# Optimization experiments

Measured on AMD Instinct MI355X. Metric: run time of the kernel, lower is better.

Reference implementation:

```python
import jax, jax.numpy as jnp
import numpy as np

B, NEG = 4, 33          # queries, candidates per query
N, R = 10000, 256       # entities, relation types (even; R//2 direct)
D, L = 64, 6            # hidden dim, conv layers
E, ER = 200000, 80000   # entity edges, edges per relation graph (hh/ht/th/tt)
F = 2 * D
EPS = 1e-5


def _ln(x, s, b):
    m = jnp.mean(x, -1, keepdims=True)
    v = jnp.mean((x - m) ** 2, -1, keepdims=True)
    return (x - m) * jax.lax.rsqrt(v + EPS) * s + b


def _conv(x, boundary, relation, src, dst, etype, p):
    # GeneralizedRelationalConv (dependent=False, project_relations=True):
    # distmult message, sum aggregate + boundary self-loop, update=relu(LN(Linear([x,agg])))
    p1w, p1b, p2w, p2b, lw, lb, lns, lnb = p
    rel = jax.nn.relu(relation @ p1w + p1b) @ p2w + p2b     # relation projection MLP
    msg = x[:, src, :] * rel[:, etype, :]                   # [B, Eg, D] gathered messages
    agg = jnp.zeros_like(boundary).at[:, dst, :].add(msg) + boundary
    out = jnp.concatenate([x, agg], -1) @ lw + lb
    return jax.nn.relu(_ln(out, lns, lnb))


def _entity_bf(rel_reps, h0, r0, src, dst, etype, params):
    # NBFNet Bellman-Ford over the entity graph, query-conditioned boundary
    q = rel_reps[jnp.arange(B), r0]                         # [B, D]
    boundary = jnp.zeros((B, N, D), q.dtype).at[jnp.arange(B), h0].add(q)
    x = boundary
    for i in range(L):
        x = _conv(x, boundary, rel_reps, src, dst, etype,
                  tuple(t[i] for t in params)) + x          # short_cut residual
    nq = jnp.broadcast_to(q[:, None, :], (B, N, D))
    return jnp.concatenate([x, nq], -1)                     # [B, N, 2D]


def _forward(floats, ints):
    (e1p1w, e1p1b, e1p2w, e1p2b, e1lw, e1lb, e1lns, e1lnb,
     e2p1w, e2p1b, e2p2w, e2p2b, e2lw, e2lb, e2lns, e2lnb,
     e2m1w, e2m1b, e2m2w, e2m2b,
     rp1w, rp1b, rp2w, rp2b, rlw, rlb, rlns, rlnb, nmw, nmb) = floats
    edge_src, edge_dst, edge_type, rel_src, rel_dst, rel_etype, batch = ints
    h0 = batch[:, 0, 0]
    t_idx = batch[:, :, 1]
    r0 = batch[:, 0, 2]
    e1p = (e1p1w, e1p1b, e1p2w, e1p2b, e1lw, e1lb, e1lns, e1lnb)
    # ---- RelNet over the 4 relation graphs (nodes=relations, edge types=entities) ----
    node_reps = jnp.ones((B, N, D), e1p1w.dtype)
    q = jnp.ones((B, D), e1p1w.dtype)
    boundary = jnp.zeros((B, R, D), q.dtype).at[jnp.arange(B), r0].add(q)
    x = boundary
    for i in range(L):
        h = sum(_conv(x, boundary, node_reps, rel_src[g], rel_dst[g], rel_etype[g],
                      (rp1w[g, i], rp1b[g, i], rp2w[g, i], rp2b[g, i],
                       rlw[g, i], rlb[g, i], rlns[g, i], rlnb[g, i]))
                for g in range(4))
        x = h + x                                           # short_cut
        if i == 0:
            # entity_model_1 refreshes the per-entity (relation-graph edge type) reps
            feat = _entity_bf(x, h0, r0, edge_src, edge_dst, edge_type, e1p)
            node_reps = feat @ nmw + nmb                    # [B, N, D]
    rel_reps = x                                            # [B, R, D]
    # ---- EntityNet 2: score candidates ----
    e2p = (e2p1w, e2p1b, e2p2w, e2p2b, e2lw, e2lb, e2lns, e2lnb)
    feat2 = _entity_bf(rel_reps, h0, r0, edge_src, edge_dst, edge_type, e2p)
    g = jnp.take_along_axis(feat2, jnp.broadcast_to(t_idx[:, :, None], (B, NEG, F)), axis=1)
    score = (jax.nn.relu(g @ e2m1w + e2m1b) @ e2m2w + e2m2b)[..., 0]
    return score                                            # [B, NEG]


def setup_inputs():
    key = jax.random.key(0)
    ks = iter(jax.random.split(key, 64))
    def w(shape, std=0.08):
        return jax.random.normal(next(ks), shape, jnp.float32) * std
    inp = {}
    inp["edge_src"] = jax.random.randint(next(ks), (E,), 0, N, jnp.int32)
    inp["edge_dst"] = jax.random.randint(next(ks), (E,), 0, N, jnp.int32)
    inp["edge_type"] = jax.random.randint(next(ks), (E,), 0, R, jnp.int32)
    inp["rel_src"] = jax.random.randint(next(ks), (4, ER), 0, R, jnp.int32)
    inp["rel_dst"] = jax.random.randint(next(ks), (4, ER), 0, R, jnp.int32)
    inp["rel_etype"] = jax.random.randint(next(ks), (4, ER), 0, N, jnp.int32)
    h = jax.random.randint(next(ks), (B, 1), 0, N, jnp.int32)
    t = jax.random.randint(next(ks), (B, NEG), 0, N, jnp.int32)
    r = jax.random.randint(next(ks), (B, 1), 0, R // 2, jnp.int32)
    inp["batch"] = jnp.stack([jnp.broadcast_to(h, (B, NEG)), t,
                              jnp.broadcast_to(r, (B, NEG))], -1)
    for pre in ("e1", "e2"):
        inp[pre + "p1w"] = w((L, D, D)); inp[pre + "p1b"] = jnp.zeros((L, D))
        inp[pre + "p2w"] = w((L, D, D)); inp[pre + "p2b"] = jnp.zeros((L, D))
        inp[pre + "lw"] = w((L, F, D));  inp[pre + "lb"] = jnp.zeros((L, D))
        inp[pre + "lns"] = jnp.ones((L, D)); inp[pre + "lnb"] = jnp.zeros((L, D))
    inp["e2m1w"] = w((F, F)); inp["e2m1b"] = jnp.zeros((F,))
    inp["e2m2w"] = w((F, 1)); inp["e2m2b"] = jnp.zeros((1,))
    inp["rp1w"] = w((4, L, D, D)); inp["rp1b"] = jnp.zeros((4, L, D))
    inp["rp2w"] = w((4, L, D, D)); inp["rp2b"] = jnp.zeros((4, L, D))
    inp["rlw"] = w((4, L, F, D));  inp["rlb"] = jnp.zeros((4, L, D))
    inp["rlns"] = jnp.ones((4, L, D)); inp["rlnb"] = jnp.zeros((4, L, D))
    inp["nmw"] = w((F, D)); inp["nmb"] = jnp.zeros((D,))
    return inp


def reference(e1p1w, e1p1b, e1p2w, e1p2b, e1lw, e1lb, e1lns, e1lnb,
              e2p1w, e2p1b, e2p2w, e2p2b, e2lw, e2lb, e2lns, e2lnb,
              e2m1w, e2m1b, e2m2w, e2m2b,
              rp1w, rp1b, rp2w, rp2b, rlw, rlb, rlns, rlnb, nmw, nmb,
              edge_src, edge_dst, edge_type, rel_src, rel_dst, rel_etype, batch):
    floats = (e1p1w, e1p1b, e1p2w, e1p2b, e1lw, e1lb, e1lns, e1lnb,
              e2p1w, e2p1b, e2p2w, e2p2b, e2lw, e2lb, e2lns, e2lnb,
              e2m1w, e2m1b, e2m2w, e2m2b,
              rp1w, rp1b, rp2w, rp2b, rlw, rlb, rlns, rlnb, nmw, nmb)
    ints = (edge_src, edge_dst, edge_type, rel_src, rel_dst, rel_etype, batch)
    return _forward(floats, ints)
```

## Files before the change

kernel.cpp:

```cpp
#include <hip/hip_runtime.h>

constexpr int kB   = 4;
constexpr int kNEG = 33;
constexpr int kN   = 10000;
constexpr int kR   = 256;
constexpr int kD   = 64;
constexpr int kL   = 6;
constexpr int kE   = 200000;
constexpr int kER  = 80000;

typedef const float* fp;
typedef __attribute__((ext_vector_type(8))) short bf16x8;
typedef __attribute__((ext_vector_type(4))) float f32x4;

__device__ __forceinline__ float rdlane(float v, int l) {
  return __uint_as_float(__builtin_amdgcn_readlane(__float_as_uint(v), l));
}
__device__ __forceinline__ float wave_sum64(float v) {
  #pragma unroll
  for (int o = 32; o > 0; o >>= 1) v += __shfl_xor(v, o, 64);
  return v;
}
__device__ __forceinline__ short f2bf(float x) {
  unsigned u = __float_as_uint(x);
  unsigned r = (u + 0x7fffu + ((u >> 16) & 1u)) >> 16;
  return (short)r;
}
__device__ __forceinline__ float bf2f_u(unsigned short s) {
  return __uint_as_float(((unsigned)s) << 16);
}
__device__ __forceinline__ float bf2f(short s) { return bf2f_u((unsigned short)s); }

__global__ void k_fill(float* __restrict__ p, float v, int n) {
  int i = blockIdx.x * blockDim.x + threadIdx.x;
  int stride = gridDim.x * blockDim.x;
  for (; i < n; i += stride) p[i] = v;
}
__global__ void k_zero_i(int* __restrict__ p, int n) {
  int i = blockIdx.x * blockDim.x + threadIdx.x;
  int stride = gridDim.x * blockDim.x;
  for (; i < n; i += stride) p[i] = 0;
}
__global__ void k_add_row(float* __restrict__ dst, const int* __restrict__ batch) {
  int tid = threadIdx.x;
  int b = tid >> 6, d = tid & 63;
  int row = batch[b * kNEG * 3 + 2];
  dst[((size_t)b * kR + row) * 64 + d] += 1.0f;
}
__global__ void k_get_q(float* __restrict__ q, const float* __restrict__ relx,
                        const int* __restrict__ batch) {
  int tid = threadIdx.x;
  int b = tid >> 6, d = tid & 63;
  int r0 = batch[b * kNEG * 3 + 2];
  q[b * 64 + d] = relx[((size_t)b * kR + r0) * 64 + d];
}

__global__ void k_hist(const int* __restrict__ dst, int ne, int* __restrict__ cnt) {
  int i = blockIdx.x * blockDim.x + threadIdx.x;
  if (i < ne) atomicAdd(&cnt[dst[i]], 1);
}
__global__ void k_hist_rel(const int* __restrict__ rel_dst, int* __restrict__ cnt) {
  int g = blockIdx.y;
  int i = blockIdx.x * blockDim.x + threadIdx.x;
  if (i < kER) atomicAdd(&cnt[g * 256 + rel_dst[(size_t)g * kER + i]], 1);
}
__global__ void k_scan_multi(const int* __restrict__ cnt, int* __restrict__ start,
                             int* __restrict__ cursor, int n, int cstride, int sstride) {
  const int* c = cnt + (size_t)blockIdx.x * cstride;
  int* st = start + (size_t)blockIdx.x * sstride;
  int* cu = cursor + (size_t)blockIdx.x * sstride;
  __shared__ int part[256];
  int t = threadIdx.x;
  int chunk = (n + 255) / 256;
  int lo = t * chunk, hi = min(lo + chunk, n);
  int s = 0;
  for (int i = lo; i < hi; ++i) s += c[i];
  part[t] = s;
  __syncthreads();
  if (t == 0) { int run = 0; for (int i = 0; i < 256; ++i) { int v = part[i]; part[i] = run; run += v; } }
  __syncthreads();
  int run = part[t];
  for (int i = lo; i < hi; ++i) { st[i] = run; cu[i] = run; run += c[i]; }
  if (t == 255) st[n] = run;
}
__global__ void k_fill_csr(const int* __restrict__ src, const int* __restrict__ dst,
                           const int* __restrict__ et, int ne,
                           int* __restrict__ cursor, int2* __restrict__ out) {
  int i = blockIdx.x * blockDim.x + threadIdx.x;
  if (i < ne) {
    int p = atomicAdd(&cursor[dst[i]], 1);
    out[p] = make_int2(src[i], et[i]);
  }
}
__global__ void k_fill_csr_rel(const int* __restrict__ src, const int* __restrict__ dst,
                               const int* __restrict__ et,
                               int* __restrict__ cursor, int2* __restrict__ out) {
  int g = blockIdx.y;
  int i = blockIdx.x * blockDim.x + threadIdx.x;
  if (i < kER) {
    int p = atomicAdd(&cursor[g * 257 + dst[(size_t)g * kER + i]], 1);
    out[(size_t)g * kER + p] = make_int2(src[(size_t)g * kER + i], et[(size_t)g * kER + i]);
  }
}

__global__ void k_packw(const float* __restrict__ w1, const float* __restrict__ w2,
                        short* __restrict__ w1h, short* __restrict__ w1l,
                        short* __restrict__ w2h, short* __restrict__ w2l) {
  int pg = blockIdx.x;
  for (int i = threadIdx.x; i < 4096; i += 256) {
    int t = i & 7, lane = (i >> 3) & 63, nt = (i >> 9) & 3, ks = i >> 11;
    int mr = lane & 15, kg = lane >> 4;
    int src = pg * 4096 + (ks * 32 + kg * 8 + t) * 64 + nt * 16 + mr;
    int dst = pg * 4096 + i;
    float v1 = w1[src]; short h1 = f2bf(v1);
    w1h[dst] = h1; w1l[dst] = f2bf(v1 - bf2f(h1));
    float v2 = w2[src]; short h2 = f2bf(v2);
    w2h[dst] = h2; w2l[dst] = f2bf(v2 - bf2f(h2));
  }
}

__global__ void __launch_bounds__(256) k_mlp_mfma(
    const float* __restrict__ in, const short* __restrict__ w1h, const short* __restrict__ w1l,
    const float* __restrict__ b1, const short* __restrict__ w2h, const short* __restrict__ w2l,
    const float* __restrict__ b2, int layer, unsigned short* __restrict__ out) {
  int g = blockIdx.y;
  int pg = g * kL + layer;
  int w = threadIdx.x >> 6, lane = threadIdx.x & 63;
  int mrow = lane & 15, kgrp = lane >> 4;
  int r0 = blockIdx.x * 64 + w * 16;
  __shared__ float hbuf[4][16][68];
  const float* xp = in + (size_t)(r0 + mrow) * 64 + kgrp * 8;
  bf16x8 a1h[2], a1l[2];
  #pragma unroll
  for (int ks = 0; ks < 2; ++ks) {
    #pragma unroll
    for (int t = 0; t < 8; ++t) {
      float v = xp[ks * 32 + t];
      short h = f2bf(v); a1h[ks][t] = h; a1l[ks][t] = f2bf(v - bf2f(h));
    }
  }
  const bf16x8* B1h = (const bf16x8*)(w1h + (size_t)pg * 4096);
  const bf16x8* B1l = (const bf16x8*)(w1l + (size_t)pg * 4096);
  #pragma unroll
  for (int nt = 0; nt < 4; ++nt) {
    f32x4 c = {0.f, 0.f, 0.f, 0.f};
    #pragma unroll
    for (int ks = 0; ks < 2; ++ks) {
      bf16x8 bh = B1h[(ks * 4 + nt) * 64 + lane];
      bf16x8 bl = B1l[(ks * 4 + nt) * 64 + lane];
      c = __builtin_amdgcn_mfma_f32_16x16x32_bf16(a1h[ks], bh, c, 0, 0, 0);
      c = __builtin_amdgcn_mfma_f32_16x16x32_bf16(a1h[ks], bl, c, 0, 0, 0);
      c = __builtin_amdgcn_mfma_f32_16x16x32_bf16(a1l[ks], bh, c, 0, 0, 0);
    }
    int col = nt * 16 + mrow;
    float bv = b1[pg * 64 + col];
    #pragma unroll
    for (int rg = 0; rg < 4; ++rg)
      hbuf[w][kgrp * 4 + rg][col] = fmaxf(c[rg] + bv, 0.f);
  }
  __syncthreads();
  bf16x8 a2h[2], a2l[2];
  #pragma unroll
  for (int ks = 0; ks < 2; ++ks) {
    #pragma unroll
    for (int t = 0; t < 8; ++t) {
      float v = hbuf[w][mrow][ks * 32 + kgrp * 8 + t];
      short h = f2bf(v); a2h[ks][t] = h; a2l[ks][t] = f2bf(v - bf2f(h));
    }
  }
  const bf16x8* B2h = (const bf16x8*)(w2h + (size_t)pg * 4096);
  const bf16x8* B2l = (const bf16x8*)(w2l + (size_t)pg * 4096);
  unsigned short* ob = out + (size_t)g * kB * kN * 64;
  #pragma unroll
  for (int nt = 0; nt < 4; ++nt) {
    f32x4 c = {0.f, 0.f, 0.f, 0.f};
    #pragma unroll
    for (int ks = 0; ks < 2; ++ks) {
      bf16x8 bh = B2h[(ks * 4 + nt) * 64 + lane];
      bf16x8 bl = B2l[(ks * 4 + nt) * 64 + lane];
      c = __builtin_amdgcn_mfma_f32_16x16x32_bf16(a2h[ks], bh, c, 0, 0, 0);
      c = __builtin_amdgcn_mfma_f32_16x16x32_bf16(a2h[ks], bl, c, 0, 0, 0);
      c = __builtin_amdgcn_mfma_f32_16x16x32_bf16(a2l[ks], bh, c, 0, 0, 0);
    }
    int col = nt * 16 + mrow;
    float bv = b2[pg * 64 + col];
    #pragma unroll
    for (int rg = 0; rg < 4; ++rg)
      ob[(size_t)(r0 + kgrp * 4 + rg) * 64 + col] = (unsigned short)f2bf(c[rg] + bv);
  }
}

__global__ void __launch_bounds__(256) k_mlp_rel6(
    const float* __restrict__ in, fp p1w, fp p1b, fp p2w, fp p2b,
    float* __restrict__ out) {
  int j = blockIdx.y;
  int row = blockIdx.x * 4 + (threadIdx.x >> 6);
  int lane = threadIdx.x & 63;
  fp W1 = p1w + (size_t)j * 4096;
  fp W2 = p2w + (size_t)j * 4096;
  float xv = in[(size_t)row * 64 + lane];
  float a = p1b[j * 64 + lane];
  float wbuf[8];
  #pragma unroll
  for (int kk = 0; kk < 64; kk += 8) {
    #pragma unroll
    for (int u = 0; u < 8; ++u) wbuf[u] = W1[(kk + u) * 64 + lane];
    #pragma unroll
    for (int u = 0; u < 8; ++u) a = fmaf(rdlane(xv, kk + u), wbuf[u], a);
  }
  a = fmaxf(a, 0.f);
  float c = p2b[j * 64 + lane];
  #pragma unroll
  for (int kk = 0; kk < 64; kk += 8) {
    #pragma unroll
    for (int u = 0; u < 8; ++u) wbuf[u] = W2[(kk + u) * 64 + lane];
    #pragma unroll
    for (int u = 0; u < 8; ++u) c = fmaf(rdlane(a, kk + u), wbuf[u], c);
  }
  out[((size_t)j * kB * kR + row) * 64 + lane] = c;
}

__global__ void k_gate0(fp p1w, fp p1b, fp p2w, fp p2b, float* __restrict__ gate0) {
  int g = threadIdx.x >> 6, lane = threadIdx.x & 63;
  int pg = g * kL;
  float a = p1b[pg * 64 + lane];
  #pragma unroll
  for (int k = 0; k < 64; ++k) a += p1w[(size_t)pg * 4096 + k * 64 + lane];
  a = fmaxf(a, 0.f);
  float c = p2b[pg * 64 + lane];
  #pragma unroll
  for (int k = 0; k < 64; ++k)
    c = fmaf(rdlane(a, k), p2w[(size_t)pg * 4096 + k * 64 + lane], c);
  gate0[g * 64 + lane] = c;
}
__global__ void k_rel_agg0(const int* __restrict__ rel_start, const int2* __restrict__ rel_edges,
                           const int* __restrict__ batch, const float* __restrict__ gate0,
                           float* __restrict__ agg) {
  int wid = (blockIdx.x * blockDim.x + threadIdx.x) >> 6;
  int lane = threadIdx.x & 63;
  int g = wid >> 10, rem = wid & 1023, b = rem >> 8, r = rem & 255;
  int r0 = batch[b * kNEG * 3 + 2];
  const int* start = rel_start + g * 257;
  const int2* edges = rel_edges + (size_t)g * kER;
  int s0 = start[r], s1 = start[r + 1];
  int cnt = 0;
  for (int base = s0; base < s1; base += 64) {
    int e = base + lane;
    bool m = false;
    if (e < s1) m = (edges[e].x == r0);
    cnt += (int)__popcll(__ballot(m));
  }
  agg[(size_t)wid * 64 + lane] = gate0[g * 64 + lane] * (float)cnt + ((r == r0) ? 1.f : 0.f);
}

__global__ void __launch_bounds__(256) k_gather_rel_all(
    const float* __restrict__ x, const unsigned short* __restrict__ gateN,
    const int* __restrict__ rel_start, const int2* __restrict__ rel_edges,
    const int* __restrict__ batch, float* __restrict__ agg) {
  int i = blockIdx.x;
  int s = i & 15, r = i >> 4;
  int g = s >> 2, b = s & 3;
  const unsigned short* gate = gateN + (size_t)g * kB * kN * 64;
  const int* start = rel_start + g * 257;
  const int2* edges = rel_edges + (size_t)g * kER;
  int w = threadIdx.x >> 6, lane = threadIdx.x & 63;
  const float* xb = x + (size_t)b * kR * 64 + lane;
  const unsigned short* gb = gate + (size_t)b * kN * 64 + lane;
  int s0 = start[r], s1 = start[r + 1];
  int len = s1 - s0;
  int per = (len + 3) >> 2;
  int e0 = s0 + w * per, e1 = min(e0 + per, s1);
  float acc = 0.f;
  int2 se;
  if (e0 < e1) se = edges[e0];
  for (int e = e0; e < e1; ++e) {
    int2 cur = se;
    if (e + 1 < e1) se = edges[e + 1];
    acc = fmaf(xb[(size_t)cur.x * 64], bf2f_u(gb[(size_t)cur.y * 64]), acc);
  }
  __shared__ float red[4][64];
  red[w][lane] = acc;
  __syncthreads();
  if (w == 0) {
    float a = red[0][lane] + red[1][lane] + red[2][lane] + red[3][lane];
    int r0 = batch[b * kNEG * 3 + 2];
    if (r == r0) a += 1.0f;
    agg[((size_t)g * kB * kR + b * kR + r) * 64 + lane] = a;
  }
}

__global__ void __launch_bounds__(256) k_conv_rel2(
    float* __restrict__ rel_x, const float* __restrict__ agg,
    fp rlw, fp rlb, fp rlns, fp rlnb, int layer) {
  int row = blockIdx.x;
  int g = threadIdx.x >> 6, lane = threadIdx.x & 63;
  int pg = g * kL + layer;
  float xr = rel_x[(size_t)row * 64 + lane];
  float ag = agg[((size_t)g * kB * kR + row) * 64 + lane];
  fp w1 = rlw + (size_t)pg * 8192;
  float o = rlb[pg * 64 + lane];
  float wbuf[8];
  #pragma unroll
  for (int kk = 0; kk < 128; kk += 8) {
    #pragma unroll
    for (int u = 0; u < 8; ++u) wbuf[u] = w1[(kk + u) * 64 + lane];
    #pragma unroll
    for (int u = 0; u < 8; ++u) {
      int k = kk + u;
      float xv = (k < 64) ? rdlane(xr, k) : rdlane(ag, k - 64);
      o = fmaf(xv, wbuf[u], o);
    }
  }
  float m = wave_sum64(o) * (1.f / 64.f);
  float c = o - m;
  float v = wave_sum64(c * c) * (1.f / 64.f);
  float y = fmaxf(c * rsqrtf(v + 1e-5f) * rlns[pg * 64 + lane] + rlnb[pg * 64 + lane], 0.f);
  __shared__ float red[4][64];
  red[g][lane] = y;
  __syncthreads();
  if (g == 0)
    rel_x[(size_t)row * 64 + lane] = xr + red[0][lane] + red[1][lane] + red[2][lane] + red[3][lane];
}

template<bool FIRST>
__global__ void __launch_bounds__(256) k_ent_layer2(
    const float* __restrict__ xcur, float* __restrict__ xnext,
    const unsigned short* __restrict__ xbf_cur, unsigned short* __restrict__ xbf_next,
    const float* __restrict__ gateL,
    const int* __restrict__ start, const int2* __restrict__ edges,
    const float* __restrict__ q, const int* __restrict__ batch,
    fp lw, fp lb, fp lns, fp lnb) {
  int n = (blockIdx.x * blockDim.x + threadIdx.x) >> 6;
  if (n >= kN) return;
  int lane = threadIdx.x & 63;
  int h0[4]; float qv[4];
  #pragma unroll
  for (int b = 0; b < 4; ++b) { h0[b] = batch[b * kNEG * 3]; qv[b] = q[b * 64 + lane]; }
  float a0 = 0.f, a1 = 0.f, a2 = 0.f, a3 = 0.f;
  int s0 = start[n], s1 = start[n + 1];
  int2 se;
  if (s0 < s1) se = edges[s0];
  for (int e = s0; e < s1; ++e) {
    int2 cur = se;
    if (e + 1 < s1) se = edges[e + 1];
    const float* gp = gateL + (size_t)cur.y * 64 + lane;
    if (FIRST) {
      if (cur.x == h0[0]) a0 = fmaf(qv[0], gp[0],     a0);
      if (cur.x == h0[1]) a1 = fmaf(qv[1], gp[16384], a1);
      if (cur.x == h0[2]) a2 = fmaf(qv[2], gp[32768], a2);
      if (cur.x == h0[3]) a3 = fmaf(qv[3], gp[49152], a3);
    } else {
      const unsigned short* xp = xbf_cur + (size_t)cur.x * 64 + lane;
      a0 = fmaf(bf2f_u(xp[0]),       gp[0],     a0);
      a1 = fmaf(bf2f_u(xp[640000]),  gp[16384], a1);
      a2 = fmaf(bf2f_u(xp[1280000]), gp[32768], a2);
      a3 = fmaf(bf2f_u(xp[1920000]), gp[49152], a3);
    }
  }
  if (n == h0[0]) a0 += qv[0];
  if (n == h0[1]) a1 += qv[1];
  if (n == h0[2]) a2 += qv[2];
  if (n == h0[3]) a3 += qv[3];
  float x0, x1, x2, x3;
  if (FIRST) {
    x0 = (n == h0[0]) ? qv[0] : 0.f; x1 = (n == h0[1]) ? qv[1] : 0.f;
    x2 = (n == h0[2]) ? qv[2] : 0.f; x3 = (n == h0[3]) ? qv[3] : 0.f;
  } else {
    const float* xp = xcur + (size_t)n * 64 + lane;
    x0 = xp[0]; x1 = xp[640000]; x2 = xp[1280000]; x3 = xp[1920000];
  }
  float bv = lb[lane];
  float o0 = bv, o1 = bv, o2 = bv, o3 = bv;
  float wbuf[8];
  #pragma unroll
  for (int kk = 0; kk < 128; kk += 8) {
    #pragma unroll
    for (int u = 0; u < 8; ++u) wbuf[u] = lw[(kk + u) * 64 + lane];
    #pragma unroll
    for (int u = 0; u < 8; ++u) {
      int k = kk + u; float w = wbuf[u];
      if (k < 64) {
        o0 = fmaf(rdlane(x0, k), w, o0); o1 = fmaf(rdlane(x1, k), w, o1);
        o2 = fmaf(rdlane(x2, k), w, o2); o3 = fmaf(rdlane(x3, k), w, o3);
      } else {
        o0 = fmaf(rdlane(a0, k - 64), w, o0); o1 = fmaf(rdlane(a1, k - 64), w, o1);
        o2 = fmaf(rdlane(a2, k - 64), w, o2); o3 = fmaf(rdlane(a3, k - 64), w, o3);
      }
    }
  }
  float s = lns[lane], t = lnb[lane];
  float* yp = xnext + (size_t)n * 64 + lane;
  unsigned short* mp = xbf_next + (size_t)n * 64 + lane;
  { float m = wave_sum64(o0) * (1.f/64.f); float c = o0 - m;
    float v = wave_sum64(c*c) * (1.f/64.f);
    float y = x0 + fmaxf(c * rsqrtf(v + 1e-5f) * s + t, 0.f);
    yp[0] = y; mp[0] = (unsigned short)f2bf(y); }
  { float m = wave_sum64(o1) * (1.f/64.f); float c = o1 - m;
    float v = wave_sum64(c*c) * (1.f/64.f);
    float y = x1 + fmaxf(c * rsqrtf(v + 1e-5f) * s + t, 0.f);
    yp[640000] = y; mp[640000] = (unsigned short)f2bf(y); }
  { float m = wave_sum64(o2) * (1.f/64.f); float c = o2 - m;
    float v = wave_sum64(c*c) * (1.f/64.f);
    float y = x2 + fmaxf(c * rsqrtf(v + 1e-5f) * s + t, 0.f);
    yp[1280000] = y; mp[1280000] = (unsigned short)f2bf(y); }
  { float m = wave_sum64(o3) * (1.f/64.f); float c = o3 - m;
    float v = wave_sum64(c*c) * (1.f/64.f);
    float y = x3 + fmaxf(c * rsqrtf(v + 1e-5f) * s + t, 0.f);
    yp[1920000] = y; mp[1920000] = (unsigned short)f2bf(y); }
}

__global__ void __launch_bounds__(256) k_nodeup4(
    const float* __restrict__ x, const float* __restrict__ q,
    fp nmw, fp nmb, float* __restrict__ out) {
  int wid = (blockIdx.x * blockDim.x + threadIdx.x) >> 6;
  int lane = threadIdx.x & 63;
  int r0 = wid * 4;
  if (r0 >= kB * kN) return;
  int b = r0 / kN;
  const float* ip = x + (size_t)r0 * 64 + lane;
  float x0 = ip[0], x1 = ip[64], x2 = ip[128], x3 = ip[192];
  float qv = q[b * 64 + lane];
  float bv = nmb[lane];
  float c0 = bv, c1 = bv, c2 = bv, c3 = bv;
  float wbuf[4];
  #pragma unroll
  for (int kk = 0; kk < 64; kk += 4) {
    #pragma unroll
    for (int u = 0; u < 4; ++u) wbuf[u] = nmw[(kk + u) * 64 + lane];
    #pragma unroll
    for (int u = 0; u < 4; ++u) {
      int k = kk + u; float w = wbuf[u];
      c0 = fmaf(rdlane(x0, k), w, c0); c1 = fmaf(rdlane(x1, k), w, c1);
      c2 = fmaf(rdlane(x2, k), w, c2); c3 = fmaf(rdlane(x3, k), w, c3);
    }
  }
  float qa = 0.f;
  #pragma unroll
  for (int k = 0; k < 64; ++k)
    qa = fmaf(rdlane(qv, k), nmw[(64 + k) * 64 + lane], qa);
  float* op = out + (size_t)r0 * 64 + lane;
  op[0] = c0 + qa; op[64] = c1 + qa; op[128] = c2 + qa; op[192] = c3 + qa;
}

__global__ void k_score(const float* __restrict__ entx, const float* __restrict__ q,
                        const int* __restrict__ batch,
                        fp m1w, fp m1b, fp m2w, fp m2b,
                        float* __restrict__ out) {
  int b = blockIdx.x / kNEG, n = blockIdx.x % kNEG;
  int t = batch[(b * kNEG + n) * 3 + 1];
  int j = threadIdx.x;
  __shared__ float gv[128];
  __shared__ float red[2];
  gv[j] = (j < 64) ? entx[((size_t)b * kN + t) * 64 + j] : q[b * 64 + (j - 64)];
  __syncthreads();
  float acc = m1b[j];
  #pragma unroll 16
  for (int k = 0; k < 128; ++k)
    acc = fmaf(gv[k], m1w[k * 128 + j], acc);
  float h = fmaxf(acc, 0.f) * m2w[j];
  h = wave_sum64(h);
  if ((j & 63) == 0) red[j >> 6] = h;
  __syncthreads();
  if (j == 0) out[b * kNEG + n] = red[0] + red[1] + m2b[0];
}

extern "C" void kernel_launch(void* const* d_in, const int* in_sizes, int n_in,
                              void* d_out, int out_size, void* d_ws, size_t ws_size,
                              hipStream_t stream) {
  const int* edge_src  = (const int*)d_in[0];
  const int* edge_dst  = (const int*)d_in[1];
  const int* edge_type = (const int*)d_in[2];
  const int* rel_src   = (const int*)d_in[3];
  const int* rel_dst   = (const int*)d_in[4];
  const int* rel_etype = (const int*)d_in[5];
  const int* batch     = (const int*)d_in[6];
  fp e1p1w = (fp)d_in[7],  e1p1b = (fp)d_in[8],  e1p2w = (fp)d_in[9],  e1p2b = (fp)d_in[10];
  fp e1lw  = (fp)d_in[11], e1lb  = (fp)d_in[12], e1lns = (fp)d_in[13], e1lnb = (fp)d_in[14];
  fp e2p1w = (fp)d_in[15], e2p1b = (fp)d_in[16], e2p2w = (fp)d_in[17], e2p2b = (fp)d_in[18];
  fp e2lw  = (fp)d_in[19], e2lb  = (fp)d_in[20], e2lns = (fp)d_in[21], e2lnb = (fp)d_in[22];
  fp e2m1w = (fp)d_in[23], e2m1b = (fp)d_in[24], e2m2w = (fp)d_in[25], e2m2b = (fp)d_in[26];
  fp rp1w  = (fp)d_in[27], rp1b  = (fp)d_in[28], rp2w  = (fp)d_in[29], rp2b  = (fp)d_in[30];
  fp rlw   = (fp)d_in[31], rlb   = (fp)d_in[32], rlns  = (fp)d_in[33], rlnb  = (fp)d_in[34];
  fp nmw   = (fp)d_in[35], nmb   = (fp)d_in[36];

  float* ws = (float*)d_ws;
  float* rel_x     = ws;
  float* q         = rel_x + 65536;
  float* gate0     = q + 256;
  float* gateR6    = gate0 + 256;
  float* rel_agg   = gateR6 + 393216;
  float* node_reps = rel_agg + 262144;
  float* ent_xa    = node_reps + 2560000;
  float* ent_xb    = ent_xa + 2560000;
  unsigned short* gateN  = (unsigned short*)(ent_xb + 2560000);
  unsigned short* ent_ba = gateN + 10240000;
  unsigned short* ent_bb = ent_ba + 2560000;
  int*   iws       = (int*)(ent_bb + 2560000);
  int2*  ent_edges = (int2*)iws;
  int2*  rel_edges = (int2*)(iws + 400000);
  int*   ent_cnt   = iws + 400000 + 640000;
  int*   ent_start = ent_cnt + 10000;
  int*   ent_cur   = ent_start + 10001;
  int*   rel_cnt   = ent_cur + 10001;
  int*   rel_start = rel_cnt + 1024;
  int*   rel_cur   = rel_start + 1028;
  short* w1hp      = (short*)(rel_cur + 1028 + 2);
  short* w1lp      = w1hp + 98304;
  short* w2hp      = w1lp + 98304;
  short* w2lp      = w2hp + 98304;

  const int nZero = 10000 + 10001 + 10001 + 1024;
  k_zero_i<<<(nZero + 255) / 256, 256, 0, stream>>>(ent_cnt, nZero);
  k_hist<<<(kE + 255) / 256, 256, 0, stream>>>(edge_dst, kE, ent_cnt);
  k_hist_rel<<<dim3((kER + 255) / 256, 4), 256, 0, stream>>>(rel_dst, rel_cnt);
  k_scan_multi<<<1, 256, 0, stream>>>(ent_cnt, ent_start, ent_cur, 10000, 0, 0);
  k_scan_multi<<<4, 256, 0, stream>>>(rel_cnt, rel_start, rel_cur, 256, 256, 257);
  k_fill_csr<<<(kE + 255) / 256, 256, 0, stream>>>(edge_src, edge_dst, edge_type, kE, ent_cur, ent_edges);
  k_fill_csr_rel<<<dim3((kER + 255) / 256, 4), 256, 0, stream>>>(rel_src, rel_dst, rel_etype, rel_cur, rel_edges);
  k_packw<<<24, 256, 0, stream>>>(rp1w, rp2w, w1hp, w1lp, w2hp, w2lp);

  k_fill<<<256, 256, 0, stream>>>(rel_x, 0.f, kB * kR * kD);
  k_add_row<<<1, 256, 0, stream>>>(rel_x, batch);

  k_gate0<<<1, 256, 0, stream>>>(rp1w, rp1b, rp2w, rp2b, gate0);
  k_rel_agg0<<<1024, 256, 0, stream>>>(rel_start, rel_edges, batch, gate0, rel_agg);
  k_conv_rel2<<<1024, 256, 0, stream>>>(rel_x, rel_agg, rlw, rlb, rlns, rlnb, 0);

  k_get_q<<<1, 256, 0, stream>>>(q, rel_x, batch);
  k_mlp_rel6<<<dim3(256, 6), 256, 0, stream>>>(rel_x, e1p1w, e1p1b, e1p2w, e1p2b, gateR6);
  {
    float* cur = ent_xa; float* nxt = ent_xb;
    unsigned short* bcur = ent_ba; unsigned short* bnxt = ent_bb;
    for (int j = 0; j < kL; ++j) {
      const float* gL = gateR6 + (size_t)j * kB * kR * 64;
      if (j == 0)
        k_ent_layer2<true><<<2500, 256, 0, stream>>>(cur, nxt, bcur, bnxt, gL, ent_start, ent_edges, q, batch,
            e1lw + (size_t)j * 8192, e1lb + (size_t)j * 64, e1lns + (size_t)j * 64, e1lnb + (size_t)j * 64);
      else
        k_ent_layer2<false><<<2500, 256, 0, stream>>>(cur, nxt, bcur, bnxt, gL, ent_start, ent_edges, q, batch,
            e1lw + (size_t)j * 8192, e1lb + (size_t)j * 64, e1lns + (size_t)j * 64, e1lnb + (size_t)j * 64);
      float* tf = cur; cur = nxt; nxt = tf;
      unsigned short* tb = bcur; bcur = bnxt; bnxt = tb;
    }
    k_nodeup4<<<2500, 256, 0, stream>>>(cur, q, nmw, nmb, node_reps);
  }

  for (int i = 1; i < kL; ++i) {
    k_mlp_mfma<<<dim3(625, 4), 256, 0, stream>>>(node_reps, w1hp, w1lp, rp1b, w2hp, w2lp, rp2b, i, gateN);
    k_gather_rel_all<<<4096, 256, 0, stream>>>(rel_x, gateN, rel_start, rel_edges, batch, rel_agg);
    k_conv_rel2<<<1024, 256, 0, stream>>>(rel_x, rel_agg, rlw, rlb, rlns, rlnb, i);
  }

  k_get_q<<<1, 256, 0, stream>>>(q, rel_x, batch);
  k_mlp_rel6<<<dim3(256, 6), 256, 0, stream>>>(rel_x, e2p1w, e2p1b, e2p2w, e2p2b, gateR6);
  {
    float* cur = ent_xa; float* nxt = ent_xb;
    unsigned short* bcur = ent_ba; unsigned short* bnxt = ent_bb;
    for (int j = 0; j < kL; ++j) {
      const float* gL = gateR6 + (size_t)j * kB * kR * 64;
      if (j == 0)
        k_ent_layer2<true><<<2500, 256, 0, stream>>>(cur, nxt, bcur, bnxt, gL, ent_start, ent_edges, q, batch,
            e2lw + (size_t)j * 8192, e2lb + (size_t)j * 64, e2lns + (size_t)j * 64, e2lnb + (size_t)j * 64);
      else
        k_ent_layer2<false><<<2500, 256, 0, stream>>>(cur, nxt, bcur, bnxt, gL, ent_start, ent_edges, q, batch,
            e2lw + (size_t)j * 8192, e2lb + (size_t)j * 64, e2lns + (size_t)j * 64, e2lnb + (size_t)j * 64);
      float* tf = cur; cur = nxt; nxt = tf;
      unsigned short* tb = bcur; bcur = bnxt; bnxt = tb;
    }
    k_score<<<kB * kNEG, 128, 0, stream>>>(cur, q, batch, e2m1w, e2m1b, e2m2w, e2m2b, (float*)d_out);
  }
}
```

Before: 1.198 ms.

## Interleave batch dimension in gathered tensors and store relation gates as bf16

The gathered operands (the entity bf16 mirror, the per-layer relation gates, the relation-net gate outputs and a new relation-state mirror) are switched from batch-major to node-major layout with the 4 batch rows adjacent. One edge gather then touches a single contiguous 512-byte or 1 KB region instead of four regions far apart. The relation gather kernel now handles all four batches per block, which cuts its grid from 4096 to 1024 blocks and removes repeated edge-list reads. The entity gates are also stored as bf16, which adds rounding error. Keeping the batch-interleaved relation-state mirror costs an extra write in the conv kernel, and the unused k_mirror_relx kernel is added but never launched.

```diff
diff --git a/kernel.cpp b/kernel.cpp
--- a/kernel.cpp
+++ b/kernel.cpp
@@ -46,6 +46,11 @@
   int b = tid >> 6, d = tid & 63;
   int row = batch[b * kNEG * 3 + 2];
   dst[((size_t)b * kR + row) * 64 + d] += 1.0f;
+}
+__global__ void k_mirror_relx(const float* __restrict__ rel_x, float* __restrict__ rxi) {
+  int i = blockIdx.x * blockDim.x + threadIdx.x;
+  int d = i & 63, r = (i >> 6) & 255, b = i >> 14;
+  rxi[((size_t)r * 4 + b) * 64 + d] = rel_x[i];
 }
 __global__ void k_get_q(float* __restrict__ q, const float* __restrict__ relx,
                         const int* __restrict__ batch) {
@@ -185,14 +190,18 @@
     int col = nt * 16 + mrow;
     float bv = b2[pg * 64 + col];
     #pragma unroll
-    for (int rg = 0; rg < 4; ++rg)
-      ob[(size_t)(r0 + kgrp * 4 + rg) * 64 + col] = (unsigned short)f2bf(c[rg] + bv);
+    for (int rg = 0; rg < 4; ++rg) {
+      int grow = r0 + kgrp * 4 + rg;
+      int bb = grow / kN;
+      int nn = grow - bb * kN;
+      ob[((size_t)nn * 4 + bb) * 64 + col] = (unsigned short)f2bf(c[rg] + bv);
+    }
   }
 }
 
 __global__ void __launch_bounds__(256) k_mlp_rel6(
     const float* __restrict__ in, fp p1w, fp p1b, fp p2w, fp p2b,
-    float* __restrict__ out) {
+    unsigned short* __restrict__ out) {
   int j = blockIdx.y;
   int row = blockIdx.x * 4 + (threadIdx.x >> 6);
   int lane = threadIdx.x & 63;
@@ -217,7 +226,8 @@
     #pragma unroll
     for (int u = 0; u < 8; ++u) c = fmaf(rdlane(a, kk + u), wbuf[u], c);
   }
-  out[((size_t)j * kB * kR + row) * 64 + lane] = c;
+  int b = row >> 8, r = row & 255;
+  out[(((size_t)j * kR + r) * 4 + b) * 64 + lane] = (unsigned short)f2bf(c);
 }
 
 __global__ void k_gate0(fp p1w, fp p1b, fp p2w, fp p2b, float* __restrict__ gate0) {
@@ -254,43 +264,43 @@
 }
 
 __global__ void __launch_bounds__(256) k_gather_rel_all(
-    const float* __restrict__ x, const unsigned short* __restrict__ gateN,
+    const float* __restrict__ rxi, const unsigned short* __restrict__ gateN,
     const int* __restrict__ rel_start, const int2* __restrict__ rel_edges,
     const int* __restrict__ batch, float* __restrict__ agg) {
   int i = blockIdx.x;
-  int s = i & 15, r = i >> 4;
-  int g = s >> 2, b = s & 3;
+  int g = i & 3, r = i >> 2;
   const unsigned short* gate = gateN + (size_t)g * kB * kN * 64;
   const int* start = rel_start + g * 257;
   const int2* edges = rel_edges + (size_t)g * kER;
   int w = threadIdx.x >> 6, lane = threadIdx.x & 63;
-  const float* xb = x + (size_t)b * kR * 64 + lane;
-  const unsigned short* gb = gate + (size_t)b * kN * 64 + lane;
   int s0 = start[r], s1 = start[r + 1];
   int len = s1 - s0;
   int per = (len + 3) >> 2;
   int e0 = s0 + w * per, e1 = min(e0 + per, s1);
-  float acc = 0.f;
+  float a0 = 0.f, a1 = 0.f, a2 = 0.f, a3 = 0.f;
   int2 se;
   if (e0 < e1) se = edges[e0];
   for (int e = e0; e < e1; ++e) {
     int2 cur = se;
     if (e + 1 < e1) se = edges[e + 1];
-    acc = fmaf(xb[(size_t)cur.x * 64], bf2f_u(gb[(size_t)cur.y * 64]), acc);
-  }
-  __shared__ float red[4][64];
-  red[w][lane] = acc;
-  __syncthreads();
-  if (w == 0) {
-    float a = red[0][lane] + red[1][lane] + red[2][lane] + red[3][lane];
-    int r0 = batch[b * kNEG * 3 + 2];
-    if (r == r0) a += 1.0f;
-    agg[((size_t)g * kB * kR + b * kR + r) * 64 + lane] = a;
-  }
+    const float* xp = rxi + (size_t)cur.x * 256 + lane;
+    const unsigned short* gp = gate + (size_t)cur.y * 256 + lane;
+    a0 = fmaf(xp[0],   bf2f_u(gp[0]),   a0);
+    a1 = fmaf(xp[64],  bf2f_u(gp[64]),  a1);
+    a2 = fmaf(xp[128], bf2f_u(gp[128]), a2);
+    a3 = fmaf(xp[192], bf2f_u(gp[192]), a3);
+  }
+  __shared__ float red[4][4][64];
+  red[w][0][lane] = a0; red[w][1][lane] = a1; red[w][2][lane] = a2; red[w][3][lane] = a3;
+  __syncthreads();
+  float a = red[0][w][lane] + red[1][w][lane] + red[2][w][lane] + red[3][w][lane];
+  int r0b = batch[w * kNEG * 3 + 2];
+  if (r == r0b) a += 1.0f;
+  agg[(((size_t)g * kB + w) * kR + r) * 64 + lane] = a;
 }
 
 __global__ void __launch_bounds__(256) k_conv_rel2(
-    float* __restrict__ rel_x, const float* __restrict__ agg,
+    float* __restrict__ rel_x, float* __restrict__ rxi, const float* __restrict__ agg,
     fp rlw, fp rlb, fp rlns, fp rlnb, int layer) {
   int row = blockIdx.x;
   int g = threadIdx.x >> 6, lane = threadIdx.x & 63;
@@ -318,15 +328,19 @@
   __shared__ float red[4][64];
   red[g][lane] = y;
   __syncthreads();
-  if (g == 0)
-    rel_x[(size_t)row * 64 + lane] = xr + red[0][lane] + red[1][lane] + red[2][lane] + red[3][lane];
+  if (g == 0) {
+    float newx = xr + red[0][lane] + red[1][lane] + red[2][lane] + red[3][lane];
+    rel_x[(size_t)row * 64 + lane] = newx;
+    int b = row >> 8, r = row & 255;
+    rxi[((size_t)r * 4 + b) * 64 + lane] = newx;
+  }
 }
 
 template<bool FIRST>
 __global__ void __launch_bounds__(256) k_ent_layer2(
     const float* __restrict__ xcur, float* __restrict__ xnext,
     const unsigned short* __restrict__ xbf_cur, unsigned short* __restrict__ xbf_next,
-    const float* __restrict__ gateL,
+    const unsigned short* __restrict__ gateL,
     const int* __restrict__ start, const int2* __restrict__ edges,
     const float* __restrict__ q, const int* __restrict__ batch,
     fp lw, fp lb, fp lns, fp lnb) {
@@ -343,18 +357,18 @@
   for (int e = s0; e < s1; ++e) {
     int2 cur = se;
     if (e + 1 < s1) se = edges[e + 1];
-    const float* gp = gateL + (size_t)cur.y * 64 + lane;
+    const unsigned short* gp = gateL + (size_t)cur.y * 256 + lane;
     if (FIRST) {
-      if (cur.x == h0[0]) a0 = fmaf(qv[0], gp[0],     a0);
-      if (cur.x == h0[1]) a1 = fmaf(qv[1], gp[16384], a1);
-      if (cur.x == h0[2]) a2 = fmaf(qv[2], gp[32768], a2);
-      if (cur.x == h0[3]) a3 = fmaf(qv[3], gp[49152], a3);
+      if (cur.x == h0[0]) a0 = fmaf(qv[0], bf2f_u(gp[0]),   a0);
+      if (cur.x == h0[1]) a1 = fmaf(qv[1], bf2f_u(gp[64]),  a1);
+      if (cur.x == h0[2]) a2 = fmaf(qv[2], bf2f_u(gp[128]), a2);
+      if (cur.x == h0[3]) a3 = fmaf(qv[3], bf2f_u(gp[192]), a3);
     } else {
-      const unsigned short* xp = xbf_cur + (size_t)cur.x * 64 + lane;
-      a0 = fmaf(bf2f_u(xp[0]),       gp[0],     a0);
-      a1 = fmaf(bf2f_u(xp[640000]),  gp[16384], a1);
-      a2 = fmaf(bf2f_u(xp[1280000]), gp[32768], a2);
-      a3 = fmaf(bf2f_u(xp[1920000]), gp[49152], a3);
+      const unsigned short* xp = xbf_cur + (size_t)cur.x * 256 + lane;
+      a0 = fmaf(bf2f_u(xp[0]),   bf2f_u(gp[0]),   a0);
+      a1 = fmaf(bf2f_u(xp[64]),  bf2f_u(gp[64]),  a1);
+      a2 = fmaf(bf2f_u(xp[128]), bf2f_u(gp[128]), a2);
+      a3 = fmaf(bf2f_u(xp[192]), bf2f_u(gp[192]), a3);
     }
   }
   if (n == h0[0]) a0 += qv[0];
@@ -390,7 +404,7 @@
   }
   float s = lns[lane], t = lnb[lane];
   float* yp = xnext + (size_t)n * 64 + lane;
-  unsigned short* mp = xbf_next + (size_t)n * 64 + lane;
+  unsigned short* mp = xbf_next + (size_t)n * 256 + lane;
   { float m = wave_sum64(o0) * (1.f/64.f); float c = o0 - m;
     float v = wave_sum64(c*c) * (1.f/64.f);
     float y = x0 + fmaxf(c * rsqrtf(v + 1e-5f) * s + t, 0.f);
@@ -398,15 +412,15 @@
   { float m = wave_sum64(o1) * (1.f/64.f); float c = o1 - m;
     float v = wave_sum64(c*c) * (1.f/64.f);
     float y = x1 + fmaxf(c * rsqrtf(v + 1e-5f) * s + t, 0.f);
-    yp[640000] = y; mp[640000] = (unsigned short)f2bf(y); }
+    yp[640000] = y; mp[64] = (unsigned short)f2bf(y); }
   { float m = wave_sum64(o2) * (1.f/64.f); float c = o2 - m;
     float v = wave_sum64(c*c) * (1.f/64.f);
     float y = x2 + fmaxf(c * rsqrtf(v + 1e-5f) * s + t, 0.f);
-    yp[1280000] = y; mp[1280000] = (unsigned short)f2bf(y); }
+    yp[1280000] = y; mp[128] = (unsigned short)f2bf(y); }
   { float m = wave_sum64(o3) * (1.f/64.f); float c = o3 - m;
     float v = wave_sum64(c*c) * (1.f/64.f);
     float y = x3 + fmaxf(c * rsqrtf(v + 1e-5f) * s + t, 0.f);
-    yp[1920000] = y; mp[1920000] = (unsigned short)f2bf(y); }
+    yp[1920000] = y; mp[192] = (unsigned short)f2bf(y); }
 }
 
 __global__ void __launch_bounds__(256) k_nodeup4(
@@ -487,12 +501,13 @@
   float* rel_x     = ws;
   float* q         = rel_x + 65536;
   float* gate0     = q + 256;
-  float* gateR6    = gate0 + 256;
-  float* rel_agg   = gateR6 + 393216;
+  float* rxi       = gate0 + 256;
+  float* rel_agg   = rxi + 65536;
   float* node_reps = rel_agg + 262144;
   float* ent_xa    = node_reps + 2560000;
   float* ent_xb    = ent_xa + 2560000;
-  unsigned short* gateN  = (unsigned short*)(ent_xb + 2560000);
+  unsigned short* gateR6 = (unsigned short*)(ent_xb + 2560000);
+  unsigned short* gateN  = gateR6 + 393216;
   unsigned short* ent_ba = gateN + 10240000;
   unsigned short* ent_bb = ent_ba + 2560000;
   int*   iws       = (int*)(ent_bb + 2560000);
@@ -524,7 +539,7 @@
 
   k_gate0<<<1, 256, 0, stream>>>(rp1w, rp1b, rp2w, rp2b, gate0);
   k_rel_agg0<<<1024, 256, 0, stream>>>(rel_start, rel_edges, batch, gate0, rel_agg);
-  k_conv_rel2<<<1024, 256, 0, stream>>>(rel_x, rel_agg, rlw, rlb, rlns, rlnb, 0);
+  k_conv_rel2<<<1024, 256, 0, stream>>>(rel_x, rxi, rel_agg, rlw, rlb, rlns, rlnb, 0);
 
   k_get_q<<<1, 256, 0, stream>>>(q, rel_x, batch);
   k_mlp_rel6<<<dim3(256, 6), 256, 0, stream>>>(rel_x, e1p1w, e1p1b, e1p2w, e1p2b, gateR6);
@@ -532,7 +547,7 @@
     float* cur = ent_xa; float* nxt = ent_xb;
     unsigned short* bcur = ent_ba; unsigned short* bnxt = ent_bb;
     for (int j = 0; j < kL; ++j) {
-      const float* gL = gateR6 + (size_t)j * kB * kR * 64;
+      const unsigned short* gL = gateR6 + (size_t)j * kR * 4 * 64;
       if (j == 0)
         k_ent_layer2<true><<<2500, 256, 0, stream>>>(cur, nxt, bcur, bnxt, gL, ent_start, ent_edges, q, batch,
             e1lw + (size_t)j * 8192, e1lb + (size_t)j * 64, e1lns + (size_t)j * 64, e1lnb + (size_t)j * 64);
@@ -547,8 +562,8 @@
 
   for (int i = 1; i < kL; ++i) {
     k_mlp_mfma<<<dim3(625, 4), 256, 0, stream>>>(node_reps, w1hp, w1lp, rp1b, w2hp, w2lp, rp2b, i, gateN);
-    k_gather_rel_all<<<4096, 256, 0, stream>>>(rel_x, gateN, rel_start, rel_edges, batch, rel_agg);
-    k_conv_rel2<<<1024, 256, 0, stream>>>(rel_x, rel_agg, rlw, rlb, rlns, rlnb, i);
+    k_gather_rel_all<<<1024, 256, 0, stream>>>(rxi, gateN, rel_start, rel_edges, batch, rel_agg);
+    k_conv_rel2<<<1024, 256, 0, stream>>>(rel_x, rxi, rel_agg, rlw, rlb, rlns, rlnb, i);
   }
 
   k_get_q<<<1, 256, 0, stream>>>(q, rel_x, batch);
@@ -557,7 +572,7 @@
     float* cur = ent_xa; float* nxt = ent_xb;
     unsigned short* bcur = ent_ba; unsigned short* bnxt = ent_bb;
     for (int j = 0; j < kL; ++j) {
-      const float* gL = gateR6 + (size_t)j * kB * kR * 64;
+      const unsigned short* gL = gateR6 + (size_t)j * kR * 4 * 64;
       if (j == 0)
         k_ent_layer2<true><<<2500, 256, 0, stream>>>(cur, nxt, bcur, bnxt, gL, ent_start, ent_edges, q, batch,
             e2lw + (size_t)j * 8192, e2lb + (size_t)j * 64, e2lns + (size_t)j * 64, e2lnb + (size_t)j * 64);
```

Result: faster. 1.054 ms (-12.0%).
